# Optimization experiments

Measured on AMD Instinct MI355X. Metric: run time of the kernel, lower is better.

Reference implementation:

```python
import jax, jax.numpy as jnp
import numpy as np

B, C, N, T, H = 4, 128, 512, 16, 4
DK = C // H
SCALE = float(np.sqrt(DK) * 1.0)  # dk**0.5 * max(tau,1e-6), tau=1.0


def setup_inputs() -> dict:
    key = jax.random.key(0)
    ks = jax.random.split(key, 6)
    x = jax.random.normal(ks[0], (B, C, N, T), jnp.float32)
    Wq = jax.random.normal(ks[1], (C, C), jnp.float32) * (1.0 / np.sqrt(C))
    Wk = jax.random.normal(ks[2], (C, C), jnp.float32) * (1.0 / np.sqrt(C))
    # original init is identity; add tiny noise so it's not degenerate
    structural = jnp.eye(N, dtype=jnp.float32) + 0.01 * jax.random.normal(ks[3], (N, N), jnp.float32)
    fusion_w = jax.random.normal(ks[4], (2,), jnp.float32) * 0.5  # 1x1 conv over 2 input channels
    fusion_b = (jax.random.normal(ks[5], (), jnp.float32) * 0.1)
    return {"x": x, "Wq": Wq, "Wk": Wk, "structural": structural,
            "fusion_w": fusion_w, "fusion_b": fusion_b}


def reference(x, Wq, Wk, structural, fusion_w, fusion_b):
    # x: [B, C, N, T]. 1x1 conv == per-channel linear; arrange to [B,T,N,H,DK]
    Q = jnp.einsum('oc,bcnt->btno', Wq, x).reshape(B, T, N, H, DK)
    K = jnp.einsum('oc,bcnt->btno', Wk, x).reshape(B, T, N, H, DK)
    # scores: [B, T, H, N, N]
    scores = jnp.einsum('btnhd,btmhd->bthnm', Q, K) / SCALE
    att_node = jax.nn.softmax(scores, axis=-1).mean(axis=(1, 2))  # [B, N, N]
    att_struct = jax.nn.softmax(structural, axis=-1)              # [N, N]
    # fusion conv (1x1, 2->1 channels) == weighted sum + bias
    fused = fusion_w[0] * att_node + fusion_w[1] * att_struct[None] + fusion_b
    fused = 0.5 * (fused + jnp.swapaxes(fused, 1, 2))  # symmetrize
    fused = jax.nn.softmax(fused, axis=-1)             # normalize='softmax'
    x_bt = jnp.transpose(x, (0, 3, 2, 1))              # [B, T, N, C]
    x_att = jnp.einsum('bij,btjc->btic', fused, x_bt)  # weighted aggregation over nodes
    return jnp.transpose(x_att, (0, 3, 2, 1))          # [B, C, N, T]
```

## Files before the change

kernel.cpp:

```cpp
#include <hip/hip_runtime.h>

#define BB 4
#define CC 128
#define NN 512
#define TT 16
#define HH 4
#define DKK 32
#define INV_SCALE 0.17677669529663687f

typedef __attribute__((ext_vector_type(8))) short bf16x8;
typedef __attribute__((ext_vector_type(4))) float f32x4;

__device__ __forceinline__ unsigned int pk2bf(float a, float b) {
  unsigned int ua = __float_as_uint(a);
  ua = (ua + 0x7FFFu + ((ua >> 16) & 1u)) >> 16;
  unsigned int ub = __float_as_uint(b);
  ub = (ub + 0x7FFFu + ((ub >> 16) & 1u)) >> 16;
  return ua | (ub << 16);
}

__device__ __forceinline__ ushort cv1(float f) {
  unsigned int u = __float_as_uint(f);
  return (ushort)((u + 0x7FFFu + ((u >> 16) & 1u)) >> 16);
}

__device__ __forceinline__ unsigned int pkfast(float a, float b) {
  unsigned int au = __float_as_uint(a) + 0x8000u;
  unsigned int bu = __float_as_uint(b) + 0x8000u;
  return __builtin_amdgcn_perm(bu, au, 0x07060302u);
}

__global__ __launch_bounds__(256) void k_wconv(const float* __restrict__ Wq,
                                               const float* __restrict__ Wk,
                                               ushort* __restrict__ Wqb,
                                               ushort* __restrict__ Wkb) {
  const int gid = blockIdx.x * 256 + threadIdx.x;
  const int i = gid * 4;
  const float* src = (i < 16384) ? (Wq + i) : (Wk + i - 16384);
  ushort* dst = (i < 16384) ? (Wqb + i) : (Wkb + i - 16384);
  float4 v = *(const float4*)src;
  uint2 u;
  u.x = pk2bf(v.x, v.y);
  u.y = pk2bf(v.z, v.w);
  *(uint2*)dst = u;
}

__global__ __launch_bounds__(256) void k_proj(const float* __restrict__ x,
                                              const ushort* __restrict__ Wqb,
                                              const ushort* __restrict__ Wkb,
                                              ushort* __restrict__ Qb,
                                              ushort* __restrict__ Kb) {
  __shared__ float xl[128 * 128];
  const int b = blockIdx.y;
  const int nt0 = blockIdx.x * 128;
  const int tid = threadIdx.x;
  const int w = tid >> 6, lane = tid & 63;
  const int lm = lane & 15, quad = lane >> 4;

  const float* xb = x + (size_t)b * 1048576 + nt0;
#pragma unroll
  for (int L = tid * 4; L < 16384; L += 1024) {
    int c = L >> 7, j = L & 127;
    *(float4*)(xl + L) = *(const float4*)(xb + c * 8192 + j);
  }

  const int o0 = w * 32;
  bf16x8 aq[2][4], ak[2][4];
#pragma unroll
  for (int ot = 0; ot < 2; ++ot)
#pragma unroll
    for (int kc = 0; kc < 4; ++kc) {
      int off = (o0 + ot * 16 + lm) * 128 + kc * 32 + quad * 8;
      aq[ot][kc] = *(const bf16x8*)(Wqb + off);
      ak[ot][kc] = *(const bf16x8*)(Wkb + off);
    }
  __syncthreads();

  const int nq = nt0 >> 4;
#pragma unroll 2
  for (int jt = 0; jt < 8; ++jt) {
    bf16x8 bfr[4];
#pragma unroll
    for (int kc = 0; kc < 4; ++kc) {
      const float* sp = xl + (kc * 32 + quad * 8) * 128 + jt * 16 + lm;
      float f0 = sp[0],   f1 = sp[128], f2 = sp[256], f3 = sp[384];
      float f4 = sp[512], f5 = sp[640], f6 = sp[768], f7 = sp[896];
      uint4 u;
      u.x = pkfast(f0, f1);
      u.y = pkfast(f2, f3);
      u.z = pkfast(f4, f5);
      u.w = pkfast(f6, f7);
      union { uint4 u; bf16x8 v; } cv;
      cv.u = u;
      bfr[kc] = cv.v;
    }

    f32x4 accq0 = {0,0,0,0}, accq1 = {0,0,0,0};
    f32x4 acck0 = {0,0,0,0}, acck1 = {0,0,0,0};
#pragma unroll
    for (int kc = 0; kc < 4; ++kc) {
      accq0 = __builtin_amdgcn_mfma_f32_16x16x32_bf16(aq[0][kc], bfr[kc], accq0, 0, 0, 0);
      accq1 = __builtin_amdgcn_mfma_f32_16x16x32_bf16(aq[1][kc], bfr[kc], accq1, 0, 0, 0);
      acck0 = __builtin_amdgcn_mfma_f32_16x16x32_bf16(ak[0][kc], bfr[kc], acck0, 0, 0, 0);
      acck1 = __builtin_amdgcn_mfma_f32_16x16x32_bf16(ak[1][kc], bfr[kc], acck1, 0, 0, 0);
    }

    const size_t base = (size_t)b * 1048576 + (size_t)lm * 65536 + w * 16384 +
                        (size_t)(nq + jt) * 32 + quad * 4;
    uint2 uq0, uq1, uk0, uk1;
    uq0.x = pk2bf(accq0[0], accq0[1]); uq0.y = pk2bf(accq0[2], accq0[3]);
    uq1.x = pk2bf(accq1[0], accq1[1]); uq1.y = pk2bf(accq1[2], accq1[3]);
    uk0.x = pk2bf(acck0[0], acck0[1]); uk0.y = pk2bf(acck0[2], acck0[3]);
    uk1.x = pk2bf(acck1[0], acck1[1]); uk1.y = pk2bf(acck1[2], acck1[3]);
    *(uint2*)(Qb + base)      = uq0;
    *(uint2*)(Qb + base + 16) = uq1;
    *(uint2*)(Kb + base)      = uk0;
    *(uint2*)(Kb + base + 16) = uk1;
  }
}

__global__ __launch_bounds__(256, 4) void k_scores(const ushort* __restrict__ Qb,
                                                   const ushort* __restrict__ Kb,
                                                   ushort* __restrict__ part) {
  __shared__ float SH[16 * 516];
  __shared__ float red[2][4][16];
  const int strip = blockIdx.x, g = blockIdx.y, b = blockIdx.z;
  const int tid = threadIdx.x;
  const int w = tid >> 6, lane = tid & 63;
  const int lm = lane & 15, quad = lane >> 4;
  const int n0 = strip * 16;
  const int wcol0 = w * 128;

  float acc[32];
#pragma unroll
  for (int i = 0; i < 32; ++i) acc[i] = 0.f;

  for (int pi = 0; pi < 8; ++pi) {
    const int p = (g << 3) + pi;
    const size_t base = (size_t)((b * 16 + (p >> 2)) * 4 + (p & 3)) * 16384;
    bf16x8 afrag = *(const bf16x8*)(Qb + base + (size_t)(n0 + lm) * 32 + quad * 8);
    bf16x8 bfr[8];
#pragma unroll
    for (int ct = 0; ct < 8; ++ct)
      bfr[ct] = *(const bf16x8*)(Kb + base + (size_t)(wcol0 + ct * 16 + lm) * 32 + quad * 8);

    f32x4 d[8];
#pragma unroll
    for (int ct = 0; ct < 8; ++ct) {
      f32x4 z = {0.f, 0.f, 0.f, 0.f};
      d[ct] = __builtin_amdgcn_mfma_f32_16x16x32_bf16(afrag, bfr[ct], z, 0, 0, 0);
    }

    float cur[32];
    float rp0 = 0.f, rp1 = 0.f, rp2 = 0.f, rp3 = 0.f;
#pragma unroll
    for (int ct = 0; ct < 8; ++ct) {
      float e0 = __expf(d[ct][0] * INV_SCALE);
      float e1 = __expf(d[ct][1] * INV_SCALE);
      float e2 = __expf(d[ct][2] * INV_SCALE);
      float e3 = __expf(d[ct][3] * INV_SCALE);
      cur[ct * 4 + 0] = e0; cur[ct * 4 + 1] = e1;
      cur[ct * 4 + 2] = e2; cur[ct * 4 + 3] = e3;
      rp0 += e0; rp1 += e1; rp2 += e2; rp3 += e3;
    }
#pragma unroll
    for (int m = 1; m < 16; m <<= 1) {
      rp0 += __shfl_xor(rp0, m);
      rp1 += __shfl_xor(rp1, m);
      rp2 += __shfl_xor(rp2, m);
      rp3 += __shfl_xor(rp3, m);
    }
    if (lm == 0) {
      red[pi & 1][w][quad * 4 + 0] = rp0;
      red[pi & 1][w][quad * 4 + 1] = rp1;
      red[pi & 1][w][quad * 4 + 2] = rp2;
      red[pi & 1][w][quad * 4 + 3] = rp3;
    }
    __syncthreads();
#pragma unroll
    for (int r = 0; r < 4; ++r) {
      float rs = red[pi & 1][0][quad * 4 + r] + red[pi & 1][1][quad * 4 + r] +
                 red[pi & 1][2][quad * 4 + r] + red[pi & 1][3][quad * 4 + r];
      float inv = 1.0f / rs;
#pragma unroll
      for (int ct = 0; ct < 8; ++ct)
        acc[ct * 4 + r] = fmaf(cur[ct * 4 + r], inv, acc[ct * 4 + r]);
    }
  }

#pragma unroll
  for (int ct = 0; ct < 8; ++ct) {
#pragma unroll
    for (int r = 0; r < 4; ++r)
      SH[(quad * 4 + r) * 516 + wcol0 + ct * 16 + lm] = acc[ct * 4 + r];
  }
  __syncthreads();
  const int row = tid >> 4, colb = (tid & 15) * 4;
  ushort* po = part + ((size_t)((g * 4 + b) * 512 + n0 + row)) * 512 + colb;
#pragma unroll
  for (int k = 0; k < 8; ++k) {
    f32x4 v = *(const f32x4*)(SH + row * 516 + colb + k * 64);
    uint2 u;
    u.x = pk2bf(v[0], v[1]);
    u.y = pk2bf(v[2], v[3]);
    *(uint2*)(po + k * 64) = u;
  }
}

__global__ __launch_bounds__(256) void k_reduce(const ushort* __restrict__ part,
                                                float* __restrict__ accA) {
  const int gid = blockIdx.x * 256 + threadIdx.x;
  const size_t idx = (size_t)gid * 4;
  float s0 = 0.f, s1 = 0.f, s2 = 0.f, s3 = 0.f;
#pragma unroll
  for (int g = 0; g < 8; ++g) {
    ushort4 v = *(const ushort4*)(part + (size_t)g * 1048576 + idx);
    s0 += __uint_as_float((unsigned int)v.x << 16);
    s1 += __uint_as_float((unsigned int)v.y << 16);
    s2 += __uint_as_float((unsigned int)v.z << 16);
    s3 += __uint_as_float((unsigned int)v.w << 16);
  }
  float4 o = make_float4(s0, s1, s2, s3);
  *(float4*)(accA + idx) = o;
}

__global__ __launch_bounds__(256) void k_sym(float* __restrict__ accA,
                                             float* __restrict__ st) {
  __shared__ float L1[64 * 68];
  __shared__ float L2[64 * 68];
  const int z = blockIdx.y;
  float* M = (z < 4) ? (accA + (size_t)z * 262144) : st;
  int rem = blockIdx.x, ti = 0;
  for (;;) { int cnt = 8 - ti; if (rem < cnt) break; rem -= cnt; ++ti; }
  const int tj = ti + rem;
  const bool diag = (ti == tj);
  const int tid = threadIdx.x;

#pragma unroll
  for (int it = 0; it < 4; ++it) {
    int L = tid * 4 + it * 1024;
    int r = L >> 6, c = L & 63;
    *(float4*)(L1 + r * 68 + c) = *(const float4*)(M + (ti * 64 + r) * 512 + tj * 64 + c);
    if (!diag)
      *(float4*)(L2 + r * 68 + c) = *(const float4*)(M + (tj * 64 + r) * 512 + ti * 64 + c);
  }
  __syncthreads();

  const float* LT = diag ? L1 : L2;
#pragma unroll
  for (int it = 0; it < 4; ++it) {
    int L = tid * 4 + it * 1024;
    int r = L >> 6, c = L & 63;
    float4 o1;
    o1.x = L1[r * 68 + c + 0] + LT[(c + 0) * 68 + r];
    o1.y = L1[r * 68 + c + 1] + LT[(c + 1) * 68 + r];
    o1.z = L1[r * 68 + c + 2] + LT[(c + 2) * 68 + r];
    o1.w = L1[r * 68 + c + 3] + LT[(c + 3) * 68 + r];
    *(float4*)(M + (ti * 64 + r) * 512 + tj * 64 + c) = o1;
    if (!diag) {
      float4 o2;
      o2.x = L2[r * 68 + c + 0] + L1[(c + 0) * 68 + r];
      o2.y = L2[r * 68 + c + 1] + L1[(c + 1) * 68 + r];
      o2.z = L2[r * 68 + c + 2] + L1[(c + 2) * 68 + r];
      o2.w = L2[r * 68 + c + 3] + L1[(c + 3) * 68 + r];
      *(float4*)(M + (tj * 64 + r) * 512 + ti * 64 + c) = o2;
    }
  }
}

__global__ __launch_bounds__(256) void k_xconv(const float* __restrict__ x,
                                               ushort* __restrict__ xtb) {
  __shared__ ushort xs[16 * 520];
  const int c = blockIdx.x, b = blockIdx.y;
  const int tid = threadIdx.x;
  const float* in = x + ((size_t)b * 128 + c) * 8192;
  ushort* outp = xtb + ((size_t)b * 128 + c) * 8192;

#pragma unroll
  for (int it = 0; it < 8; ++it) {
    int idx = (tid + it * 256) * 4;
    int j = idx >> 4, t0 = idx & 15;
    float4 v = *(const float4*)(in + idx);
    xs[(t0 + 0) * 520 + j] = cv1(v.x);
    xs[(t0 + 1) * 520 + j] = cv1(v.y);
    xs[(t0 + 2) * 520 + j] = cv1(v.z);
    xs[(t0 + 3) * 520 + j] = cv1(v.w);
  }
  __syncthreads();
#pragma unroll
  for (int it = 0; it < 4; ++it) {
    int u = (tid + it * 256) * 8;
    int t = u >> 9, j0 = u & 511;
    *(uint4*)(outp + u) = *(const uint4*)(xs + t * 520 + j0);
  }
}

__device__ __forceinline__ float blk_max(float v, float* red, int tid) {
#pragma unroll
  for (int off = 32; off > 0; off >>= 1) v = fmaxf(v, __shfl_xor(v, off, 64));
  if ((tid & 63) == 0) red[tid >> 6] = v;
  __syncthreads();
  v = fmaxf(fmaxf(red[0], red[1]), fmaxf(red[2], red[3]));
  __syncthreads();
  return v;
}
__device__ __forceinline__ float blk_sum(float v, float* red, int tid) {
#pragma unroll
  for (int off = 32; off > 0; off >>= 1) v += __shfl_xor(v, off, 64);
  if ((tid & 63) == 0) red[tid >> 6] = v;
  __syncthreads();
  v = (red[0] + red[1]) + (red[2] + red[3]);
  __syncthreads();
  return v;
}

__global__ __launch_bounds__(256) void k_struct(const float* __restrict__ S,
                                                float* __restrict__ st) {
  __shared__ float red[4];
  const int i = blockIdx.x, tid = threadIdx.x;
  float s0 = S[i * 512 + tid], s1 = S[i * 512 + tid + 256];
  float m = blk_max(fmaxf(s0, s1), red, tid);
  float e0 = __expf(s0 - m), e1 = __expf(s1 - m);
  float sum = blk_sum(e0 + e1, red, tid);
  float inv = 1.0f / sum;
  st[i * 512 + tid] = e0 * inv;
  st[i * 512 + tid + 256] = e1 * inv;
}

__global__ __launch_bounds__(256) void k_fused(const float* __restrict__ accA,
                                               const float* __restrict__ st,
                                               const float* __restrict__ fw,
                                               const float* __restrict__ fb,
                                               ushort* __restrict__ fusedb) {
  __shared__ float red[4];
  const int i = blockIdx.x, b = blockIdx.y, tid = threadIdx.x;
  const float w0s = fw[0] * (0.5f / 64.f);
  const float w1s = fw[1] * 0.5f;
  const float bias = fb[0];
  const float* A = accA + (size_t)b * 262144 + (size_t)i * 512;
  const float* S = st + (size_t)i * 512;
  float2 a2 = *(const float2*)(A + tid * 2);
  float2 s2 = *(const float2*)(S + tid * 2);
  float l0 = fmaf(w0s, a2.x, fmaf(w1s, s2.x, bias));
  float l1 = fmaf(w0s, a2.y, fmaf(w1s, s2.y, bias));
  float m = blk_max(fmaxf(l0, l1), red, tid);
  float e0 = __expf(l0 - m), e1 = __expf(l1 - m);
  float sum = blk_sum(e0 + e1, red, tid);
  float inv = 1.0f / sum;
  *(unsigned int*)(fusedb + ((size_t)(b * 512 + i)) * 512 + tid * 2) =
      pk2bf(e0 * inv, e1 * inv);
}

__global__ __launch_bounds__(256) void k_agg(const ushort* __restrict__ fusedb,
                                             const ushort* __restrict__ xtb,
                                             float* __restrict__ out) {
  __shared__ ushort xs[16 * 520];
  const int cg = blockIdx.x;
  const int i0 = blockIdx.y * 64;
  const int b = blockIdx.z;
  const int tid = threadIdx.x, w = tid >> 6, lane = tid & 63;
  const int lm = lane & 15, quad = lane >> 4;

  const ushort* fr = fusedb + ((size_t)(b * 512 + i0 + w * 16 + lm)) * 512 + quad * 8;
  bf16x8 af[16];
#pragma unroll
  for (int kk = 0; kk < 16; ++kk) af[kk] = *(const bf16x8*)(fr + kk * 32);

  const ushort* xg = xtb + ((size_t)b * 128 + cg * 8) * 8192;
  uint4 rg[4];
#pragma unroll
  for (int it = 0; it < 4; ++it) rg[it] = *(const uint4*)(xg + (tid + it * 256) * 8);

  for (int c = 0; c < 8; ++c) {
#pragma unroll
    for (int it = 0; it < 4; ++it) {
      int u = (tid + it * 256) * 8;
      int t = u >> 9, j0 = u & 511;
      *(uint4*)(xs + t * 520 + j0) = rg[it];
    }
    __syncthreads();
    if (c < 7) {
      const ushort* xg2 = xg + (size_t)(c + 1) * 8192;
#pragma unroll
      for (int it = 0; it < 4; ++it) rg[it] = *(const uint4*)(xg2 + (tid + it * 256) * 8);
    }
    f32x4 acc = {0.f, 0.f, 0.f, 0.f};
#pragma unroll
    for (int kk = 0; kk < 16; ++kk) {
      bf16x8 bf = *(const bf16x8*)(xs + lm * 520 + kk * 32 + quad * 8);
      acc = __builtin_amdgcn_mfma_f32_16x16x32_bf16(af[kk], bf, acc, 0, 0, 0);
    }
    float* op = out + (size_t)b * 1048576 + (size_t)(cg * 8 + c) * 8192 +
                (size_t)(i0 + w * 16 + quad * 4) * 16 + lm;
    op[0]  = acc[0];
    op[16] = acc[1];
    op[32] = acc[2];
    op[48] = acc[3];
    __syncthreads();
  }
}

extern "C" void kernel_launch(void* const* d_in, const int* in_sizes, int n_in,
                              void* d_out, int out_size, void* d_ws, size_t ws_size,
                              hipStream_t stream) {
  const float* x  = (const float*)d_in[0];
  const float* Wq = (const float*)d_in[1];
  const float* Wk = (const float*)d_in[2];
  const float* S  = (const float*)d_in[3];
  const float* fw = (const float*)d_in[4];
  const float* fb = (const float*)d_in[5];
  float* out = (float*)d_out;

  ushort* Qb   = (ushort*)d_ws;
  ushort* Kb   = Qb + 4194304;
  ushort* part = Kb + 4194304;
  ushort* xtb  = (ushort*)d_ws;
  float* accA  = (float*)d_ws + 8388608;
  float* st    = accA + 1048576;
  ushort* fusedb = (ushort*)(st + 262144);
  ushort* Wqb  = fusedb + 1048576;
  ushort* Wkb  = Wqb + 16384;

  k_wconv <<<dim3(32),        256, 0, stream>>>(Wq, Wk, Wqb, Wkb);
  k_proj  <<<dim3(64, 4),     256, 0, stream>>>(x, Wqb, Wkb, Qb, Kb);
  k_scores<<<dim3(32, 8, 4),  256, 0, stream>>>(Qb, Kb, part);
  k_struct<<<dim3(512),       256, 0, stream>>>(S, st);
  k_reduce<<<dim3(1024),      256, 0, stream>>>(part, accA);
  k_sym   <<<dim3(36, 5),     256, 0, stream>>>(accA, st);
  k_xconv <<<dim3(128, 4),    256, 0, stream>>>(x, xtb);
  k_fused <<<dim3(512, 4),    256, 0, stream>>>(accA, st, fw, fb, fusedb);
  k_agg   <<<dim3(16, 8, 4),  256, 0, stream>>>(fusedb, xtb, out);
}
```

Before: 162.2 us.

## Fuse weight conversion, x transpose, reduce and symmetrize into fewer kernels

Folds the weight bf16 conversion and the 1/scale factor into the projection kernel. That kernel now also writes the transposed bf16 copy of x, so the separate xconv pass is dropped. The partial-sum reduction and symmetrization become a single kernel, and the score kernel now uses 4 partial groups instead of 8. The aim is fewer launches and less global-memory traffic from the reduce/sym round trips, at the cost of less parallelism in k_scores and more weight reloading across the doubled set of proj blocks.

```diff
diff --git a/kernel.cpp b/kernel.cpp
--- a/kernel.cpp
+++ b/kernel.cpp
@@ -6,6 +6,7 @@
 #define TT 16
 #define HH 4
 #define DKK 32
+#define GPART 4
 #define INV_SCALE 0.17677669529663687f
 
 typedef __attribute__((ext_vector_type(8))) short bf16x8;
@@ -19,49 +20,38 @@
   return ua | (ub << 16);
 }
 
-__device__ __forceinline__ ushort cv1(float f) {
-  unsigned int u = __float_as_uint(f);
-  return (ushort)((u + 0x7FFFu + ((u >> 16) & 1u)) >> 16);
-}
-
 __device__ __forceinline__ unsigned int pkfast(float a, float b) {
   unsigned int au = __float_as_uint(a) + 0x8000u;
   unsigned int bu = __float_as_uint(b) + 0x8000u;
   return __builtin_amdgcn_perm(bu, au, 0x07060302u);
 }
 
-__global__ __launch_bounds__(256) void k_wconv(const float* __restrict__ Wq,
-                                               const float* __restrict__ Wk,
-                                               ushort* __restrict__ Wqb,
-                                               ushort* __restrict__ Wkb) {
-  const int gid = blockIdx.x * 256 + threadIdx.x;
-  const int i = gid * 4;
-  const float* src = (i < 16384) ? (Wq + i) : (Wk + i - 16384);
-  ushort* dst = (i < 16384) ? (Wqb + i) : (Wkb + i - 16384);
-  float4 v = *(const float4*)src;
-  uint2 u;
-  u.x = pk2bf(v.x, v.y);
-  u.y = pk2bf(v.z, v.w);
-  *(uint2*)dst = u;
+__device__ __forceinline__ float bf2f(ushort v) {
+  return __uint_as_float((unsigned int)v << 16);
 }
 
 __global__ __launch_bounds__(256) void k_proj(const float* __restrict__ x,
-                                              const ushort* __restrict__ Wqb,
-                                              const ushort* __restrict__ Wkb,
+                                              const float* __restrict__ Wq,
+                                              const float* __restrict__ Wk,
                                               ushort* __restrict__ Qb,
-                                              ushort* __restrict__ Kb) {
-  __shared__ float xl[128 * 128];
+                                              ushort* __restrict__ Kb,
+                                              ushort* __restrict__ xtb) {
+  __shared__ float xl[128 * 66];
   const int b = blockIdx.y;
-  const int nt0 = blockIdx.x * 128;
+  const int nt0 = blockIdx.x * 64;
+  const int nq = nt0 >> 4;
   const int tid = threadIdx.x;
   const int w = tid >> 6, lane = tid & 63;
   const int lm = lane & 15, quad = lane >> 4;
 
   const float* xb = x + (size_t)b * 1048576 + nt0;
 #pragma unroll
-  for (int L = tid * 4; L < 16384; L += 1024) {
-    int c = L >> 7, j = L & 127;
-    *(float4*)(xl + L) = *(const float4*)(xb + c * 8192 + j);
+  for (int L = tid * 4; L < 8192; L += 1024) {
+    int c = L >> 6, j = L & 63;
+    float4 v = *(const float4*)(xb + c * 8192 + j);
+    float2* dp = (float2*)(xl + c * 66 + j);
+    dp[0] = make_float2(v.x, v.y);
+    dp[1] = make_float2(v.z, v.w);
   }
 
   const int o0 = w * 32;
@@ -70,28 +60,38 @@
   for (int ot = 0; ot < 2; ++ot)
 #pragma unroll
     for (int kc = 0; kc < 4; ++kc) {
-      int off = (o0 + ot * 16 + lm) * 128 + kc * 32 + quad * 8;
-      aq[ot][kc] = *(const bf16x8*)(Wqb + off);
-      ak[ot][kc] = *(const bf16x8*)(Wkb + off);
-    }
-  __syncthreads();
-
-  const int nq = nt0 >> 4;
-#pragma unroll 2
-  for (int jt = 0; jt < 8; ++jt) {
+      const int off = (o0 + ot * 16 + lm) * 128 + kc * 32 + quad * 8;
+      const float4 q1 = *(const float4*)(Wq + off);
+      const float4 q2 = *(const float4*)(Wq + off + 4);
+      const float4 k1 = *(const float4*)(Wk + off);
+      const float4 k2 = *(const float4*)(Wk + off + 4);
+      union { uint4 u; bf16x8 v; } cq, ck;
+      cq.u.x = pk2bf(q1.x * INV_SCALE, q1.y * INV_SCALE);
+      cq.u.y = pk2bf(q1.z * INV_SCALE, q1.w * INV_SCALE);
+      cq.u.z = pk2bf(q2.x * INV_SCALE, q2.y * INV_SCALE);
+      cq.u.w = pk2bf(q2.z * INV_SCALE, q2.w * INV_SCALE);
+      ck.u.x = pk2bf(k1.x, k1.y);
+      ck.u.y = pk2bf(k1.z, k1.w);
+      ck.u.z = pk2bf(k2.x, k2.y);
+      ck.u.w = pk2bf(k2.z, k2.w);
+      aq[ot][kc] = cq.v;
+      ak[ot][kc] = ck.v;
+    }
+  __syncthreads();
+
+#pragma unroll
+  for (int jtl = 0; jtl < 4; ++jtl) {
     bf16x8 bfr[4];
 #pragma unroll
     for (int kc = 0; kc < 4; ++kc) {
-      const float* sp = xl + (kc * 32 + quad * 8) * 128 + jt * 16 + lm;
-      float f0 = sp[0],   f1 = sp[128], f2 = sp[256], f3 = sp[384];
-      float f4 = sp[512], f5 = sp[640], f6 = sp[768], f7 = sp[896];
-      uint4 u;
-      u.x = pkfast(f0, f1);
-      u.y = pkfast(f2, f3);
-      u.z = pkfast(f4, f5);
-      u.w = pkfast(f6, f7);
+      const float* sp = xl + (kc * 32 + quad * 8) * 66 + jtl * 16 + lm;
+      float f0 = sp[0],   f1 = sp[66],  f2 = sp[132], f3 = sp[198];
+      float f4 = sp[264], f5 = sp[330], f6 = sp[396], f7 = sp[462];
       union { uint4 u; bf16x8 v; } cv;
-      cv.u = u;
+      cv.u.x = pkfast(f0, f1);
+      cv.u.y = pkfast(f2, f3);
+      cv.u.z = pkfast(f4, f5);
+      cv.u.w = pkfast(f6, f7);
       bfr[kc] = cv.v;
     }
 
@@ -106,7 +106,7 @@
     }
 
     const size_t base = (size_t)b * 1048576 + (size_t)lm * 65536 + w * 16384 +
-                        (size_t)(nq + jt) * 32 + quad * 4;
+                        (size_t)(nq + jtl) * 32 + quad * 4;
     uint2 uq0, uq1, uk0, uk1;
     uq0.x = pk2bf(accq0[0], accq0[1]); uq0.y = pk2bf(accq0[2], accq0[3]);
     uq1.x = pk2bf(accq1[0], accq1[1]); uq1.y = pk2bf(accq1[2], accq1[3]);
@@ -116,6 +116,18 @@
     *(uint2*)(Qb + base + 16) = uq1;
     *(uint2*)(Kb + base)      = uk0;
     *(uint2*)(Kb + base + 16) = uk1;
+  }
+
+  const int tloc = tid & 15, c0 = (tid >> 4) * 8;
+  ushort* xo = xtb + ((size_t)b * 128) * 8192;
+#pragma unroll
+  for (int s = 0; s < 8; ++s) {
+    const int c = c0 + s;
+    const float* sp = xl + c * 66 + tloc;
+    uint2 u;
+    u.x = pk2bf(sp[0], sp[16]);
+    u.y = pk2bf(sp[32], sp[48]);
+    *(uint2*)(xo + (size_t)c * 8192 + tloc * 512 + nq) = u;
   }
 }
 
@@ -135,8 +147,8 @@
 #pragma unroll
   for (int i = 0; i < 32; ++i) acc[i] = 0.f;
 
-  for (int pi = 0; pi < 8; ++pi) {
-    const int p = (g << 3) + pi;
+  for (int pi = 0; pi < 16; ++pi) {
+    const int p = g * 16 + pi;
     const size_t base = (size_t)((b * 16 + (p >> 2)) * 4 + (p & 3)) * 16384;
     bf16x8 afrag = *(const bf16x8*)(Qb + base + (size_t)(n0 + lm) * 32 + quad * 8);
     bf16x8 bfr[8];
@@ -155,10 +167,10 @@
     float rp0 = 0.f, rp1 = 0.f, rp2 = 0.f, rp3 = 0.f;
 #pragma unroll
     for (int ct = 0; ct < 8; ++ct) {
-      float e0 = __expf(d[ct][0] * INV_SCALE);
-      float e1 = __expf(d[ct][1] * INV_SCALE);
-      float e2 = __expf(d[ct][2] * INV_SCALE);
-      float e3 = __expf(d[ct][3] * INV_SCALE);
+      float e0 = __expf(d[ct][0]);
+      float e1 = __expf(d[ct][1]);
+      float e2 = __expf(d[ct][2]);
+      float e3 = __expf(d[ct][3]);
       cur[ct * 4 + 0] = e0; cur[ct * 4 + 1] = e1;
       cur[ct * 4 + 2] = e2; cur[ct * 4 + 3] = e3;
       rp0 += e0; rp1 += e1; rp2 += e2; rp3 += e3;
@@ -204,94 +216,6 @@
     u.x = pk2bf(v[0], v[1]);
     u.y = pk2bf(v[2], v[3]);
     *(uint2*)(po + k * 64) = u;
-  }
-}
-
-__global__ __launch_bounds__(256) void k_reduce(const ushort* __restrict__ part,
-                                                float* __restrict__ accA) {
-  const int gid = blockIdx.x * 256 + threadIdx.x;
-  const size_t idx = (size_t)gid * 4;
-  float s0 = 0.f, s1 = 0.f, s2 = 0.f, s3 = 0.f;
-#pragma unroll
-  for (int g = 0; g < 8; ++g) {
-    ushort4 v = *(const ushort4*)(part + (size_t)g * 1048576 + idx);
-    s0 += __uint_as_float((unsigned int)v.x << 16);
-    s1 += __uint_as_float((unsigned int)v.y << 16);
-    s2 += __uint_as_float((unsigned int)v.z << 16);
-    s3 += __uint_as_float((unsigned int)v.w << 16);
-  }
-  float4 o = make_float4(s0, s1, s2, s3);
-  *(float4*)(accA + idx) = o;
-}
-
-__global__ __launch_bounds__(256) void k_sym(float* __restrict__ accA,
-                                             float* __restrict__ st) {
-  __shared__ float L1[64 * 68];
-  __shared__ float L2[64 * 68];
-  const int z = blockIdx.y;
-  float* M = (z < 4) ? (accA + (size_t)z * 262144) : st;
-  int rem = blockIdx.x, ti = 0;
-  for (;;) { int cnt = 8 - ti; if (rem < cnt) break; rem -= cnt; ++ti; }
-  const int tj = ti + rem;
-  const bool diag = (ti == tj);
-  const int tid = threadIdx.x;
-
-#pragma unroll
-  for (int it = 0; it < 4; ++it) {
-    int L = tid * 4 + it * 1024;
-    int r = L >> 6, c = L & 63;
-    *(float4*)(L1 + r * 68 + c) = *(const float4*)(M + (ti * 64 + r) * 512 + tj * 64 + c);
-    if (!diag)
-      *(float4*)(L2 + r * 68 + c) = *(const float4*)(M + (tj * 64 + r) * 512 + ti * 64 + c);
-  }
-  __syncthreads();
-
-  const float* LT = diag ? L1 : L2;
-#pragma unroll
-  for (int it = 0; it < 4; ++it) {
-    int L = tid * 4 + it * 1024;
-    int r = L >> 6, c = L & 63;
-    float4 o1;
-    o1.x = L1[r * 68 + c + 0] + LT[(c + 0) * 68 + r];
-    o1.y = L1[r * 68 + c + 1] + LT[(c + 1) * 68 + r];
-    o1.z = L1[r * 68 + c + 2] + LT[(c + 2) * 68 + r];
-    o1.w = L1[r * 68 + c + 3] + LT[(c + 3) * 68 + r];
-    *(float4*)(M + (ti * 64 + r) * 512 + tj * 64 + c) = o1;
-    if (!diag) {
-      float4 o2;
-      o2.x = L2[r * 68 + c + 0] + L1[(c + 0) * 68 + r];
-      o2.y = L2[r * 68 + c + 1] + L1[(c + 1) * 68 + r];
-      o2.z = L2[r * 68 + c + 2] + L1[(c + 2) * 68 + r];
-      o2.w = L2[r * 68 + c + 3] + L1[(c + 3) * 68 + r];
-      *(float4*)(M + (tj * 64 + r) * 512 + ti * 64 + c) = o2;
-    }
-  }
-}
-
-__global__ __launch_bounds__(256) void k_xconv(const float* __restrict__ x,
-                                               ushort* __restrict__ xtb) {
-  __shared__ ushort xs[16 * 520];
-  const int c = blockIdx.x, b = blockIdx.y;
-  const int tid = threadIdx.x;
-  const float* in = x + ((size_t)b * 128 + c) * 8192;
-  ushort* outp = xtb + ((size_t)b * 128 + c) * 8192;
-
-#pragma unroll
-  for (int it = 0; it < 8; ++it) {
-    int idx = (tid + it * 256) * 4;
-    int j = idx >> 4, t0 = idx & 15;
-    float4 v = *(const float4*)(in + idx);
-    xs[(t0 + 0) * 520 + j] = cv1(v.x);
-    xs[(t0 + 1) * 520 + j] = cv1(v.y);
-    xs[(t0 + 2) * 520 + j] = cv1(v.z);
-    xs[(t0 + 3) * 520 + j] = cv1(v.w);
-  }
-  __syncthreads();
-#pragma unroll
-  for (int it = 0; it < 4; ++it) {
-    int u = (tid + it * 256) * 8;
-    int t = u >> 9, j0 = u & 511;
-    *(uint4*)(outp + u) = *(const uint4*)(xs + t * 520 + j0);
   }
 }
 
@@ -327,7 +251,94 @@
   st[i * 512 + tid + 256] = e1 * inv;
 }
 
-__global__ __launch_bounds__(256) void k_fused(const float* __restrict__ accA,
+__global__ __launch_bounds__(256) void k_redsym(const ushort* __restrict__ part,
+                                                float* __restrict__ Ssym,
+                                                float* __restrict__ st) {
+  __shared__ float L1[64 * 68];
+  __shared__ float L2[64 * 68];
+  const int z = blockIdx.y;
+  int rem = blockIdx.x, ti = 0;
+  for (;;) { int cnt = 8 - ti; if (rem < cnt) break; rem -= cnt; ++ti; }
+  const int tj = ti + rem;
+  const bool diag = (ti == tj);
+  const int tid = threadIdx.x;
+  const int rr = tid >> 2, cc = (tid & 3) * 16;
+
+  float a1[16], a2[16];
+#pragma unroll
+  for (int k = 0; k < 16; ++k) { a1[k] = 0.f; a2[k] = 0.f; }
+
+  if (z == 4) {
+    const float* p1 = st + (ti * 64 + rr) * 512 + tj * 64 + cc;
+    const float* p2 = st + (tj * 64 + rr) * 512 + ti * 64 + cc;
+#pragma unroll
+    for (int q = 0; q < 4; ++q) {
+      float4 v = *(const float4*)(p1 + q * 4);
+      a1[q * 4 + 0] = v.x; a1[q * 4 + 1] = v.y;
+      a1[q * 4 + 2] = v.z; a1[q * 4 + 3] = v.w;
+      if (!diag) {
+        float4 u = *(const float4*)(p2 + q * 4);
+        a2[q * 4 + 0] = u.x; a2[q * 4 + 1] = u.y;
+        a2[q * 4 + 2] = u.z; a2[q * 4 + 3] = u.w;
+      }
+    }
+  } else {
+    const int b = z;
+#pragma unroll
+    for (int g = 0; g < GPART; ++g) {
+      const ushort* p1 = part + ((size_t)((g * 4 + b) * 512 + ti * 64 + rr)) * 512 + tj * 64 + cc;
+      const ushort* p2 = part + ((size_t)((g * 4 + b) * 512 + tj * 64 + rr)) * 512 + ti * 64 + cc;
+#pragma unroll
+      for (int q = 0; q < 4; ++q) {
+        ushort4 v = *(const ushort4*)(p1 + q * 4);
+        a1[q * 4 + 0] += bf2f(v.x); a1[q * 4 + 1] += bf2f(v.y);
+        a1[q * 4 + 2] += bf2f(v.z); a1[q * 4 + 3] += bf2f(v.w);
+        if (!diag) {
+          ushort4 u = *(const ushort4*)(p2 + q * 4);
+          a2[q * 4 + 0] += bf2f(u.x); a2[q * 4 + 1] += bf2f(u.y);
+          a2[q * 4 + 2] += bf2f(u.z); a2[q * 4 + 3] += bf2f(u.w);
+        }
+      }
+    }
+  }
+
+#pragma unroll
+  for (int q = 0; q < 4; ++q) {
+    *(float4*)(L1 + rr * 68 + cc + q * 4) =
+        make_float4(a1[q * 4], a1[q * 4 + 1], a1[q * 4 + 2], a1[q * 4 + 3]);
+    if (!diag)
+      *(float4*)(L2 + rr * 68 + cc + q * 4) =
+          make_float4(a2[q * 4], a2[q * 4 + 1], a2[q * 4 + 2], a2[q * 4 + 3]);
+  }
+  __syncthreads();
+
+  float* M = (z < 4) ? (Ssym + (size_t)z * 262144) : st;
+  const float* LT = diag ? L1 : L2;
+#pragma unroll
+  for (int q = 0; q < 4; ++q) {
+    const int c = cc + q * 4;
+    float4 o;
+    o.x = L1[rr * 68 + c + 0] + LT[(c + 0) * 68 + rr];
+    o.y = L1[rr * 68 + c + 1] + LT[(c + 1) * 68 + rr];
+    o.z = L1[rr * 68 + c + 2] + LT[(c + 2) * 68 + rr];
+    o.w = L1[rr * 68 + c + 3] + LT[(c + 3) * 68 + rr];
+    *(float4*)(M + (ti * 64 + rr) * 512 + tj * 64 + c) = o;
+  }
+  if (!diag) {
+#pragma unroll
+    for (int q = 0; q < 4; ++q) {
+      const int c = cc + q * 4;
+      float4 o;
+      o.x = L2[rr * 68 + c + 0] + L1[(c + 0) * 68 + rr];
+      o.y = L2[rr * 68 + c + 1] + L1[(c + 1) * 68 + rr];
+      o.z = L2[rr * 68 + c + 2] + L1[(c + 2) * 68 + rr];
+      o.w = L2[rr * 68 + c + 3] + L1[(c + 3) * 68 + rr];
+      *(float4*)(M + (tj * 64 + rr) * 512 + ti * 64 + c) = o;
+    }
+  }
+}
+
+__global__ __launch_bounds__(256) void k_fused(const float* __restrict__ Ssym,
                                                const float* __restrict__ st,
                                                const float* __restrict__ fw,
                                                const float* __restrict__ fb,
@@ -337,7 +348,7 @@
   const float w0s = fw[0] * (0.5f / 64.f);
   const float w1s = fw[1] * 0.5f;
   const float bias = fb[0];
-  const float* A = accA + (size_t)b * 262144 + (size_t)i * 512;
+  const float* A = Ssym + (size_t)b * 262144 + (size_t)i * 512;
   const float* S = st + (size_t)i * 512;
   float2 a2 = *(const float2*)(A + tid * 2);
   float2 s2 = *(const float2*)(S + tid * 2);
@@ -414,20 +425,15 @@
   ushort* Qb   = (ushort*)d_ws;
   ushort* Kb   = Qb + 4194304;
   ushort* part = Kb + 4194304;
-  ushort* xtb  = (ushort*)d_ws;
-  float* accA  = (float*)d_ws + 8388608;
-  float* st    = accA + 1048576;
+  ushort* xtb  = part + 4194304;
+  float* Ssym  = (float*)(xtb + 4194304);
+  float* st    = Ssym + 1048576;
   ushort* fusedb = (ushort*)(st + 262144);
-  ushort* Wqb  = fusedb + 1048576;
-  ushort* Wkb  = Wqb + 16384;
-
-  k_wconv <<<dim3(32),        256, 0, stream>>>(Wq, Wk, Wqb, Wkb);
-  k_proj  <<<dim3(64, 4),     256, 0, stream>>>(x, Wqb, Wkb, Qb, Kb);
-  k_scores<<<dim3(32, 8, 4),  256, 0, stream>>>(Qb, Kb, part);
-  k_struct<<<dim3(512),       256, 0, stream>>>(S, st);
-  k_reduce<<<dim3(1024),      256, 0, stream>>>(part, accA);
-  k_sym   <<<dim3(36, 5),     256, 0, stream>>>(accA, st);
-  k_xconv <<<dim3(128, 4),    256, 0, stream>>>(x, xtb);
-  k_fused <<<dim3(512, 4),    256, 0, stream>>>(accA, st, fw, fb, fusedb);
-  k_agg   <<<dim3(16, 8, 4),  256, 0, stream>>>(fusedb, xtb, out);
-}
+
+  k_proj  <<<dim3(128, 4),      256, 0, stream>>>(x, Wq, Wk, Qb, Kb, xtb);
+  k_scores<<<dim3(32, GPART, 4),256, 0, stream>>>(Qb, Kb, part);
+  k_struct<<<dim3(512),         256, 0, stream>>>(S, st);
+  k_redsym<<<dim3(36, 5),       256, 0, stream>>>(part, Ssym, st);
+  k_fused <<<dim3(512, 4),      256, 0, stream>>>(Ssym, st, fw, fb, fusedb);
+  k_agg   <<<dim3(16, 8, 4),    256, 0, stream>>>(fusedb, xtb, out);
+}
```

Measured after the change: 171.7 us. 5.9% more time.
